# Performance work log

Measured on AMD Instinct MI355X. Metric: run time of the kernel, lower is better.

The kernel has to match this reference:

```python
import jax, jax.numpy as jnp
import numpy as np
from jax import lax

N_NODES = 50000
N_EDGES = 200000
N_FEAT = 512
HIDDEN = 256
N_FILT = 4
FIND_STEPS = 18  # > log2(N_NODES); valid because union-by-size bounds tree height


def _find(parent, x):
    # pointer-jump to root; fixed trip count, root is a fixed point (parent[r]==r)
    return lax.fori_loop(0, FIND_STEPS, lambda i, y: parent[y], x)


def persistence_dim0(v, src, dst):
    """Dim-0 persistence diagram for one filtration.
    v: (N,) node filtration values. src/dst: (E,) int32 edge endpoints.
    Returns (N, 2) array of (birth, death) pairs, one per node.
    Union-find over edges sorted by filtration value max(v[u], v[w]);
    when two components merge, the younger one's minimum node dies at the edge value.
    Essential components die at max(v). The scan is purely integer-typed so the
    only differentiable path to deaths is the final gather from edge weights w.
    """
    N = v.shape[0]
    w = jnp.maximum(v[src], v[dst])  # (E,) edge filtration values
    edge_order = lax.stop_gradient(jnp.argsort(w)).astype(jnp.int32)
    vertex_order = jnp.argsort(lax.stop_gradient(v))
    rank = jnp.zeros((N,), jnp.int32).at[vertex_order].set(jnp.arange(N, dtype=jnp.int32))

    init = (
        jnp.arange(N, dtype=jnp.int32),      # parent
        jnp.ones((N,), jnp.int32),           # component size (union by size)
        rank,                                 # min birth-rank of component, stored at root
        jnp.arange(N, dtype=jnp.int32),      # node achieving min rank, stored at root
        jnp.full((N,), -1, jnp.int32),       # killing edge index per node (-1 = essential)
    )

    def step(carry, e):
        parent, size, mrank, mnode, kill = carry
        u = src[e]
        t = dst[e]
        ru = _find(parent, u)
        rt = _find(parent, t)
        merge = ru != rt
        # younger component = larger min birth-rank; its representative node dies here
        ru_young = mrank[ru] > mrank[rt]
        young = jnp.where(ru_young, ru, rt)
        kn = mnode[young]
        kill = kill.at[kn].set(jnp.where(merge, e, kill[kn]))
        # union by size: attach smaller tree under larger
        big = jnp.where(size[ru] >= size[rt], ru, rt)
        small = jnp.where(size[ru] >= size[rt], rt, ru)
        parent = parent.at[small].set(jnp.where(merge, big, parent[small]))
        size = size.at[big].set(jnp.where(merge, size[ru] + size[rt], size[big]))
        nm_rank = jnp.minimum(mrank[ru], mrank[rt])
        nm_node = jnp.where(mrank[ru] <= mrank[rt], mnode[ru], mnode[rt])
        mrank = mrank.at[big].set(jnp.where(merge, nm_rank, mrank[big]))
        mnode = mnode.at[big].set(jnp.where(merge, nm_node, mnode[big]))
        return (parent, size, mrank, mnode, kill), None

    (_, _, _, _, kill), _ = lax.scan(step, init, edge_order)
    death = jnp.where(kill >= 0, w[jnp.maximum(kill, 0)], jnp.max(v))
    return jnp.stack([v, death], axis=-1)  # (N, 2)


def setup_inputs() -> dict:
    key = jax.random.key(0)
    k1, k2, k3, k4 = jax.random.split(key, 4)
    X = jax.random.normal(k1, (N_NODES, N_FEAT), dtype=jnp.float32)
    edge_index = jax.random.randint(k2, (2, N_EDGES), 0, N_NODES, dtype=jnp.int64)
    s1 = 1.0 / np.sqrt(N_FEAT)
    s2 = 1.0 / np.sqrt(HIDDEN)
    W1 = jax.random.uniform(k3, (N_FEAT, HIDDEN), jnp.float32, -s1, s1)
    b1 = jnp.zeros((HIDDEN,), jnp.float32)
    W2 = jax.random.uniform(k4, (HIDDEN, N_FILT), jnp.float32, -s2, s2)
    b2 = jnp.zeros((N_FILT,), jnp.float32)
    return {"X": X, "W1": W1, "b1": b1, "W2": W2, "b2": b2, "edge_index": edge_index}


def reference(X, W1, b1, W2, b2, edge_index):
    # filtration MLP: Linear -> ReLU -> Linear, (n_nodes, n_filtrations)
    filt = jax.nn.relu(X @ W1 + b1) @ W2 + b2
    src = edge_index[0].astype(jnp.int32)
    dst = edge_index[1].astype(jnp.int32)
    # (n_filtrations, n_nodes, 2) dim-0 persistence diagrams
    diagrams = jax.vmap(lambda v: persistence_dim0(v, src, dst))(filt.T)
    return diagrams
```

## Files before the change

### kernel.cpp

```cpp
#include <hip/hip_runtime.h>
#include <stdint.h>

#define NN 50000
#define NE 200000
#define NFEAT 512
#define NHID 256
#define NPART 32
#define NCB 7
#define CSTEP 25000
#define NGUF 56
#define NBLKE 196
#define NBLKN 49

typedef unsigned long long u64;
typedef unsigned int u32;
typedef unsigned short u16;

__device__ const int PB[NPART + 1] = {
    0, 6272, 12544, 18816, 25088, 31360, 37632, 43904, 50176,
    56448, 62720, 68992, 75264, 81536, 87808, 94080, 100352,
    106624, 112896, 119168, 125440, 131712, 137984, 144256, 150528,
    156800, 163072, 169344, 175616, 181888, 188160, 194432, 200000};

__device__ const int GOFF[NCB + 1] = {0, 2, 6, 12, 20, 30, 42, 56};

__device__ __forceinline__ u32 encf(float x) {
  u32 u = __float_as_uint(x);
  return (u & 0x80000000u) ? ~u : (u | 0x80000000u);
}
__device__ __forceinline__ float decf(u32 y) {
  u32 u = (y & 0x80000000u) ? (y ^ 0x80000000u) : ~y;
  return __uint_as_float(u);
}

#define SWZ(c) ((c) ^ ((((c) >> 5) & 7) << 2))

__global__ __launch_bounds__(256) void mlp_kernel(
    const float* __restrict__ X, const float* __restrict__ W1,
    const float* __restrict__ b1, const float* __restrict__ W2,
    const float* __restrict__ b2, float* __restrict__ filt)
{
  __shared__ float As[64][33];
  __shared__ float Ws[32][256];
  __shared__ float W2s[256][4];

  const int tid = threadIdx.x;
  const int row0 = blockIdx.x * 64;
  const int tr = tid >> 4, tc = tid & 15;

  for (int i = tid; i < NHID * 4; i += 256) W2s[i >> 2][i & 3] = W2[i];

  float4 acc[4][4];
  #pragma unroll
  for (int i = 0; i < 4; i++)
    #pragma unroll
    for (int q = 0; q < 4; q++) acc[i][q] = make_float4(0.f, 0.f, 0.f, 0.f);

  for (int k0 = 0; k0 < NFEAT; k0 += 32) {
    __syncthreads();
    {
      const int r = tid >> 3, c4 = (tid & 7) << 2;
      #pragma unroll
      for (int rr = 0; rr < 2; rr++) {
        const int row = r + rr * 32;
        const int grow = row0 + row;
        float4 v = make_float4(0.f, 0.f, 0.f, 0.f);
        if (grow < NN) v = *(const float4*)&X[(size_t)grow * NFEAT + k0 + c4];
        As[row][c4 + 0] = v.x; As[row][c4 + 1] = v.y;
        As[row][c4 + 2] = v.z; As[row][c4 + 3] = v.w;
      }
      const int wr = tid >> 6, wc4 = (tid & 63) << 2;
      const int pc = SWZ(wc4);
      #pragma unroll
      for (int rr = 0; rr < 8; rr++) {
        const int rowk = wr + rr * 4;
        float4 v = *(const float4*)&W1[(size_t)(k0 + rowk) * NHID + wc4];
        *(float4*)&Ws[rowk][pc] = v;
      }
    }
    __syncthreads();
    #pragma unroll 8
    for (int kk = 0; kk < 32; kk++) {
      const float a0 = As[tr * 4 + 0][kk], a1 = As[tr * 4 + 1][kk],
                  a2 = As[tr * 4 + 2][kk], a3 = As[tr * 4 + 3][kk];
      #pragma unroll
      for (int q = 0; q < 4; q++) {
        const int col = tc * 16 + q * 4;
        const float4 wv = *(const float4*)&Ws[kk][SWZ(col)];
        acc[0][q].x += a0 * wv.x; acc[0][q].y += a0 * wv.y;
        acc[0][q].z += a0 * wv.z; acc[0][q].w += a0 * wv.w;
        acc[1][q].x += a1 * wv.x; acc[1][q].y += a1 * wv.y;
        acc[1][q].z += a1 * wv.z; acc[1][q].w += a1 * wv.w;
        acc[2][q].x += a2 * wv.x; acc[2][q].y += a2 * wv.y;
        acc[2][q].z += a2 * wv.z; acc[2][q].w += a2 * wv.w;
        acc[3][q].x += a3 * wv.x; acc[3][q].y += a3 * wv.y;
        acc[3][q].w += a3 * wv.w; acc[3][q].z += a3 * wv.z;
      }
    }
  }

  float p[4][4];
  #pragma unroll
  for (int i = 0; i < 4; i++)
    #pragma unroll
    for (int f = 0; f < 4; f++) p[i][f] = 0.f;

  #pragma unroll
  for (int q = 0; q < 4; q++) {
    const int colb = tc * 16 + q * 4;
    float bb[4];
    #pragma unroll
    for (int j = 0; j < 4; j++) bb[j] = b1[colb + j];
    #pragma unroll
    for (int i = 0; i < 4; i++) {
      float h[4] = {acc[i][q].x + bb[0], acc[i][q].y + bb[1],
                    acc[i][q].z + bb[2], acc[i][q].w + bb[3]};
      #pragma unroll
      for (int j = 0; j < 4; j++) {
        const float hh = fmaxf(h[j], 0.f);
        #pragma unroll
        for (int f = 0; f < 4; f++) p[i][f] += hh * W2s[colb + j][f];
      }
    }
  }

  #pragma unroll
  for (int m = 1; m < 16; m <<= 1)
    #pragma unroll
    for (int i = 0; i < 4; i++)
      #pragma unroll
      for (int f = 0; f < 4; f++)
        p[i][f] += __shfl_xor(p[i][f], m, 64);

  if (tc == 0) {
    const float c0 = b2[0], c1 = b2[1], c2 = b2[2], c3 = b2[3];
    #pragma unroll
    for (int i = 0; i < 4; i++) {
      const int row = row0 + tr * 4 + i;
      if (row < NN) {
        float4 o = make_float4(p[i][0] + c0, p[i][1] + c1, p[i][2] + c2, p[i][3] + c3);
        *(float4*)&filt[(size_t)row * 4] = o;
      }
    }
  }
}

__global__ void zero4_kernel(u32* __restrict__ maxv) {
  if (threadIdx.x < 4) maxv[threadIdx.x] = 0u;
}

__global__ __launch_bounds__(256) void maxv_kernel(const float* __restrict__ filt,
                                                   u32* __restrict__ maxv)
{
  __shared__ u32 lm[4];
  if (threadIdx.x < 4) lm[threadIdx.x] = 0u;
  __syncthreads();
  const int n = blockIdx.x * 256 + threadIdx.x;
  if (n < NN) {
    const float4 v = *(const float4*)&filt[(size_t)n * 4];
    atomicMax(&lm[0], encf(v.x));
    atomicMax(&lm[1], encf(v.y));
    atomicMax(&lm[2], encf(v.z));
    atomicMax(&lm[3], encf(v.w));
  }
  __syncthreads();
  if (threadIdx.x < 4) atomicMax(&maxv[threadIdx.x], lm[threadIdx.x]);
}

__global__ __launch_bounds__(256) void nodeprep_kernel(const float* __restrict__ filt,
                                                       u64* __restrict__ nodekeys)
{
  const int n = blockIdx.x * 256 + threadIdx.x;
  const int f = blockIdx.y;
  if (n < NN) {
    const float v = filt[(size_t)n * 4 + f];
    nodekeys[(size_t)f * NN + n] = ((u64)encf(v) << 32) | (u32)n;
  }
}

__global__ __launch_bounds__(256) void radix_hist(
    const u64* __restrict__ src, u32* __restrict__ hist, int n, int nblk, int shift)
{
  __shared__ u32 cnt[256];
  const int tid = threadIdx.x;
  const int blk = blockIdx.x;
  const int f = blockIdx.y;
  src += (size_t)f * n;
  hist += (size_t)f * 256 * nblk;
  cnt[tid] = 0;
  __syncthreads();
  #pragma unroll
  for (int k = 0; k < 4; k++) {
    const int i = blk * 1024 + k * 256 + tid;
    if (i < n) atomicAdd(&cnt[(u32)(src[i] >> shift) & 255u], 1u);
  }
  __syncthreads();
  hist[(size_t)tid * nblk + blk] = cnt[tid];
}

__global__ __launch_bounds__(256) void radix_scan_rows(
    u32* __restrict__ hist, u32* __restrict__ rowtot, int nblk)
{
  __shared__ u32 buf[256];
  const int d = blockIdx.x, f = blockIdx.y;
  const int tid = threadIdx.x;
  u32* row = hist + ((size_t)f * 256 + d) * nblk;
  u32 v = (tid < nblk) ? row[tid] : 0u;
  buf[tid] = v;
  __syncthreads();
  for (int off = 1; off < 256; off <<= 1) {
    const u32 t = (tid >= off) ? buf[tid - off] : 0u;
    __syncthreads();
    buf[tid] += t;
    __syncthreads();
  }
  if (tid < nblk) row[tid] = buf[tid] - v;
  if (tid == 255) rowtot[f * 256 + d] = buf[255];
}

__global__ __launch_bounds__(256) void radix_scan_digits(u32* __restrict__ rowtot)
{
  __shared__ u32 buf[256];
  const int f = blockIdx.x, tid = threadIdx.x;
  const u32 v = rowtot[f * 256 + tid];
  buf[tid] = v;
  __syncthreads();
  for (int off = 1; off < 256; off <<= 1) {
    const u32 t = (tid >= off) ? buf[tid - off] : 0u;
    __syncthreads();
    buf[tid] += t;
    __syncthreads();
  }
  rowtot[f * 256 + tid] = buf[tid] - v;
}

__global__ __launch_bounds__(256) void radix_scatter(
    const u64* __restrict__ src, u64* __restrict__ dst,
    const u32* __restrict__ hist, const u32* __restrict__ rowtot,
    int n, int nblk, int shift)
{
  __shared__ u32 baseD[256];
  __shared__ u32 accum[256];
  __shared__ u32 roundCnt[4 * 256];
  const int tid = threadIdx.x;
  const int blk = blockIdx.x;
  const int f = blockIdx.y;
  const int lane = tid & 63, wid = tid >> 6;
  src += (size_t)f * n;
  dst += (size_t)f * n;
  baseD[tid] = hist[(size_t)f * 256 * nblk + (size_t)tid * nblk + blk] +
               rowtot[f * 256 + tid];
  accum[tid] = 0;
  for (int k = 0; k < 4; k++) {
    roundCnt[tid] = 0; roundCnt[tid + 256] = 0;
    roundCnt[tid + 512] = 0; roundCnt[tid + 768] = 0;
    __syncthreads();
    const int i = blk * 1024 + k * 256 + tid;
    const bool valid = (i < n);
    const u64 key = valid ? src[i] : 0ull;
    const u32 d = (u32)(key >> shift) & 255u;
    u64 peers = __ballot(valid);
    #pragma unroll
    for (int b = 0; b < 8; b++) {
      const u64 bal = __ballot((d >> b) & 1u);
      peers &= ((d >> b) & 1u) ? bal : ~bal;
    }
    const u32 rank = (u32)__popcll(peers & ((1ull << lane) - 1ull));
    if (valid && (__ffsll((long long)peers) - 1 == lane))
      roundCnt[wid * 256 + d] = (u32)__popcll(peers);
    __syncthreads();
    if (valid) {
      u32 off = baseD[d] + accum[d] + rank;
      for (int w2 = 0; w2 < wid; w2++) off += roundCnt[w2 * 256 + d];
      dst[off] = key;
    }
    __syncthreads();
    accum[tid] += roundCnt[tid] + roundCnt[256 + tid] +
                  roundCnt[512 + tid] + roundCnt[768 + tid];
    __syncthreads();
  }
}

__global__ __launch_bounds__(256) void rank_kernel(const u64* __restrict__ nodekeys,
                                                   u32* __restrict__ rankOf,
                                                   u32* __restrict__ nodeOf)
{
  const int j = blockIdx.x * 256 + threadIdx.x;
  const int f = blockIdx.y;
  if (j < NN) {
    const u64 kk = nodekeys[(size_t)f * NN + j];
    const u32 node = (u32)(kk & 0xffffffffu);
    rankOf[(size_t)f * NN + node] = (u32)j;
    nodeOf[(size_t)f * NN + j] = node;
  }
}

__global__ __launch_bounds__(256) void init_kernel(
    const float* __restrict__ filt, const u32* __restrict__ maxv,
    float* __restrict__ out)
{
  const int n = blockIdx.x * 256 + threadIdx.x;
  const int f = blockIdx.y;
  if (n < NN) {
    const size_t idx = (size_t)f * NN + n;
    out[idx * 2 + 0] = filt[(size_t)n * 4 + f];
    out[idx * 2 + 1] = decf(maxv[f]);
  }
}

__global__ __launch_bounds__(256) void prep_kernel(
    const int* __restrict__ ei, const float* __restrict__ filt,
    const u32* __restrict__ rankOf, u64* __restrict__ pairs)
{
  const int e = blockIdx.x * 256 + threadIdx.x;
  if (e >= NE) return;
  const int s = ei[e];
  const int d = ei[NE + e];
  const float4 vs = *(const float4*)&filt[(size_t)s * 4];
  const float4 vd = *(const float4*)&filt[(size_t)d * 4];
  float wf[4] = {fmaxf(vs.x, vd.x), fmaxf(vs.y, vd.y),
                 fmaxf(vs.z, vd.z), fmaxf(vs.w, vd.w)};
  #pragma unroll
  for (int f = 0; f < 4; f++) {
    const u32 ru = rankOf[(size_t)f * NN + s];
    const u32 rt = rankOf[(size_t)f * NN + d];
    pairs[(size_t)f * NE + e] = ((u64)encf(wf[f]) << 32) | ((ru << 16) | rt);
  }
}

__global__ __launch_bounds__(256) void gparinit_kernel(u32* __restrict__ gpar)
{
  const int n = blockIdx.x * 256 + threadIdx.x;
  const int jf = blockIdx.y;
  if (n < NN) gpar[(size_t)jf * NN + n] = (u32)n;
}

__global__ __launch_bounds__(1024) void guf_kernel(
    const u64* __restrict__ pairs, u32* __restrict__ gpar)
{
  const int bx = blockIdx.x;
  const int f = blockIdx.y;
  int j = 0;
  while (j < NCB - 1 && bx >= GOFF[j + 1]) j++;
  const int b = bx - GOFF[j];
  const int nb = 2 * (j + 1);
  const int cb = CSTEP * (j + 1);
  const int s0 = (int)(((long long)cb * b) / nb);
  const int s1 = (int)(((long long)cb * (b + 1)) / nb);
  u32* gp = gpar + (size_t)(j * 4 + f) * NN;
  const u64* ps = pairs + (size_t)f * NE;

  for (int e = s0 + (int)threadIdx.x; e < s1; e += 1024) {
    const u32 pr = (u32)(ps[e] & 0xffffffffu);
    u32 x = pr >> 16, y = pr & 0xffffu;
    while (true) {
      u32 px = gp[x];
      while (px != x) { const u32 g = gp[px]; gp[x] = g; x = g; px = gp[x]; }
      u32 py = gp[y];
      while (py != y) { const u32 g = gp[py]; gp[y] = g; y = g; py = gp[y]; }
      if (x == y) break;
      const u32 h = (x > y) ? x : y;
      const u32 l = x ^ y ^ h;
      const u32 old = atomicCAS(&gp[h], h, l);
      if (old == h) break;
      x = old; y = l;
    }
  }
}

__global__ __launch_bounds__(1024) void uf_kernel(
    const u64* __restrict__ pairs, const u32* __restrict__ gpar,
    u64* __restrict__ qbuf, u32* __restrict__ qcnt)
{
  __shared__ __align__(16) u16 par[NN];
  __shared__ __align__(16) u32 scratch[1024];
  const int q = blockIdx.x, f = blockIdx.y;
  const int tid = threadIdx.x;
  const u64* ps = pairs + (size_t)f * NE;
  const int lo = PB[q], hi = PB[q + 1];
  int jb = lo / CSTEP; if (jb > NCB) jb = NCB;
  const int base = jb * CSTEP;

  u32* par32 = (u32*)par;
  if (jb == 0) {
    for (int j = tid; j < NN / 2; j += 1024)
      par32[j] = ((u32)(2 * j + 1) << 16) | (u32)(2 * j);
  } else {
    const u32* gp = gpar + (size_t)((jb - 1) * 4 + f) * NN;
    for (int n = tid; n < NN; n += 1024) par[n] = (u16)gp[n];
  }
  __syncthreads();

  {
    volatile u16* vpar = par;
    for (int e = base + tid; e < lo; e += 1024) {
      const u32 pr = (u32)(ps[e] & 0xffffffffu);
      u32 x = pr >> 16, y = pr & 0xffffu;
      while (true) {
        u32 px = vpar[x];
        while (px != x) { const u32 g = vpar[px]; vpar[x] = (u16)g; x = g; px = vpar[x]; }
        u32 py = vpar[y];
        while (py != y) { const u32 g = vpar[py]; vpar[y] = (u16)g; y = g; py = vpar[y]; }
        if (x == y) break;
        const u32 h = (x > y) ? x : y;
        const u32 l = x ^ y ^ h;
        volatile u32* w32 = (volatile u32*)par32 + (h >> 1);
        const bool hiH = (h & 1u) != 0u;
        bool hooked = false, lost = false;
        while (!hooked && !lost) {
          const u32 cur = *w32;
          const u32 half = hiH ? (cur >> 16) : (cur & 0xffffu);
          if (half != h) { lost = true; break; }
          const u32 nw = hiH ? ((cur & 0x0000ffffu) | (l << 16))
                             : ((cur & 0xffff0000u) | l);
          if (atomicCAS((u32*)w32, cur, nw) == cur) hooked = true;
        }
        if (hooked) break;
        x = h; y = l;
      }
    }
  }
  __syncthreads();

  if (tid >= 64) return;
  const int lane = tid;
  u64* qb = qbuf + (size_t)f * NE + lo;
  u32 qcount = 0;
  uint4* h4 = (uint4*)scratch;
  const uint4 zz = make_uint4(0u, 0u, 0u, 0u);

  u64 pair0 = ps[lo + lane];
  u64 pair1 = (lo + 64 < hi) ? ps[lo + 64 + lane] : 0ull;

  for (int base2 = lo; base2 < hi; base2 += 64) {
    u64 pair2 = 0ull;
    if (base2 + 128 < hi) pair2 = ps[base2 + 128 + lane];

    const u32 pr = (u32)(pair0 & 0xffffffffu);
    const u32 deathw = (u32)(pair0 >> 32);
    const int u = (int)(pr >> 16), t = (int)(pr & 0xffffu);

    int ru = u, rt = t;
    u32 pu = par[ru], pt = par[rt];
    while (pu != (u32)ru || pt != (u32)rt) {
      const u32 gu = par[pu];
      const u32 gt = par[pt];
      if (pu != (u32)ru) { par[ru] = (u16)gu; ru = (int)gu; }
      if (pt != (u32)rt) { par[rt] = (u16)gt; rt = (int)gt; }
      pu = par[ru]; pt = par[rt];
    }

    const bool mg = (ru != rt);
    const u32 winv = (ru < rt) ? (u32)ru : (u32)rt;
    const u32 losev = (u32)(ru ^ rt) ^ winv;
    const u64 mball = __ballot(mg);
    const int nm = (int)__popcll(mball);

    bool flag = false;
    if (nm > 1) {
      #pragma unroll
      for (int k = 0; k < 4; k++) h4[lane + 64 * k] = zz;
      const u32 hu = ((u32)ru * 2654435761u) >> 22;
      const u32 ht = ((u32)rt * 2654435761u) >> 22;
      if (mg) { atomicAdd(&scratch[hu], 1u); atomicAdd(&scratch[ht], 1u); }
      asm volatile("s_waitcnt lgkmcnt(0)" ::: "memory");
      u32 cl = 0u;
      if (mg) cl = scratch[(losev == (u32)ru) ? hu : ht];
      flag = mg && (cl >= 2u);
    }

    u32 myLose = 0xffffffffu, myWin = 0u;
    if (mg && !flag) { myLose = losev; myWin = winv; }

    u64 chain = __ballot(flag);
    u32 mp = ((u32)ru << 16) | (u32)rt;
    while (chain) {
      const int l = __ffsll((long long)chain) - 1;
      chain &= (chain - 1);
      const u32 ab = (u32)__builtin_amdgcn_readlane((int)mp, l);
      const u32 a = ab >> 16, b = ab & 0xffffu;
      if (a != b) {
        const u32 win = a < b ? a : b;
        const u32 lose = a ^ b ^ win;
        const bool isme = (lane == l);
        myLose = isme ? lose : myLose;
        myWin = isme ? win : myWin;
        const u32 h2 = mp >> 16, l2m = mp & 0xffffu;
        mp = ((h2 == lose ? win : h2) << 16) | (l2m == lose ? win : l2m);
      }
    }

    const u64 mmask = __ballot(myLose != 0xffffffffu);
    if (myLose != 0xffffffffu) {
      par[myLose] = (u16)myWin;
      const u32 idx = (u32)__popcll(mmask & ((1ull << lane) - 1ull));
      qb[qcount + idx] = ((u64)deathw << 32) | myLose;
    }
    qcount += (u32)__popcll(mmask);

    asm volatile("s_waitcnt lgkmcnt(0)" ::: "memory");
    __builtin_amdgcn_sched_barrier(0);
    pair0 = pair1; pair1 = pair2;
  }
  if (lane == 0) qcnt[f * NPART + q] = qcount;
}

__global__ __launch_bounds__(256) void finalize_kernel(
    const u64* __restrict__ qbuf, const u32* __restrict__ qcnt,
    const u32* __restrict__ nodeOf, float* __restrict__ out)
{
  const int e = blockIdx.x * 256 + threadIdx.x;
  const int f = blockIdx.y;
  if (e >= NE) return;
  int q = 0;
  while (q < NPART - 1 && e >= PB[q + 1]) q++;
  if ((u32)(e - PB[q]) < qcnt[f * NPART + q]) {
    const u64 v = qbuf[(size_t)f * NE + e];
    const u32 lose = (u32)(v & 0xffffffffu);
    const u32 node = nodeOf[(size_t)f * NN + lose];
    out[((size_t)f * NN + node) * 2 + 1] = decf((u32)(v >> 32));
  }
}

extern "C" void kernel_launch(void* const* d_in, const int* in_sizes, int n_in,
                              void* d_out, int out_size, void* d_ws, size_t ws_size,
                              hipStream_t stream)
{
  const float* X  = (const float*)d_in[0];
  const float* W1 = (const float*)d_in[1];
  const float* b1 = (const float*)d_in[2];
  const float* W2 = (const float*)d_in[3];
  const float* b2 = (const float*)d_in[4];
  const int*   EI = (const int*)d_in[5];
  float* out = (float*)d_out;

  char* w = (char*)d_ws;
  u64*  A      = (u64*)w;   w += (size_t)4 * NE * sizeof(u64);
  char* Bb     = w;         w += (size_t)4 * NE * sizeof(u64);
  u64*  qbuf   = (u64*)w;   w += (size_t)4 * NE * sizeof(u64);
  float* filt  = (float*)w; w += (size_t)NN * 4 * sizeof(float);
  u32*  rankOf = (u32*)w;   w += (size_t)4 * NN * sizeof(u32);
  u32*  nodeOf = (u32*)w;   w += (size_t)4 * NN * sizeof(u32);
  u32*  qcnt   = (u32*)w;   w += 128 * sizeof(u32);
  u32*  rowtot = (u32*)w;   w += 4 * 256 * sizeof(u32);
  u32*  maxv   = (u32*)w;   w += 4 * sizeof(u32);

  u64* NA   = (u64*)Bb;
  u64* NB   = (u64*)(Bb + 1600000);
  u64* EB   = (u64*)Bb;
  u32* gpar = (u32*)Bb;
  u32* nhist = rankOf;
  u32* ehist = (u32*)filt;

  const size_t need = (size_t)(w - (char*)d_ws);
  if (ws_size < need) return;

  const int nodeBlocks = (NN + 255) / 256;
  const int edgeBlocks = (NE + 255) / 256;

  zero4_kernel<<<dim3(1), dim3(64), 0, stream>>>(maxv);
  mlp_kernel<<<dim3((NN + 63) / 64), dim3(256), 0, stream>>>(X, W1, b1, W2, b2, filt);
  maxv_kernel<<<dim3(nodeBlocks, 1), dim3(256), 0, stream>>>(filt, maxv);
  nodeprep_kernel<<<dim3(nodeBlocks, 4), dim3(256), 0, stream>>>(filt, NA);

  {
    u64 *s = NA, *d = NB;
    for (int p = 0; p < 4; p++) {
      const int sh = 32 + 8 * p;
      radix_hist<<<dim3(NBLKN, 4), dim3(256), 0, stream>>>(s, nhist, NN, NBLKN, sh);
      radix_scan_rows<<<dim3(256, 4), dim3(256), 0, stream>>>(nhist, rowtot, NBLKN);
      radix_scan_digits<<<dim3(4), dim3(256), 0, stream>>>(rowtot);
      radix_scatter<<<dim3(NBLKN, 4), dim3(256), 0, stream>>>(s, d, nhist, rowtot,
                                                              NN, NBLKN, sh);
      u64* t = s; s = d; d = t;
    }
  }

  rank_kernel<<<dim3(nodeBlocks, 4), dim3(256), 0, stream>>>(NA, rankOf, nodeOf);
  init_kernel<<<dim3(nodeBlocks, 4), dim3(256), 0, stream>>>(filt, maxv, out);
  prep_kernel<<<dim3(edgeBlocks, 1), dim3(256), 0, stream>>>(EI, filt, rankOf, A);

  {
    u64 *s = A, *d = EB;
    for (int p = 0; p < 4; p++) {
      const int sh = 32 + 8 * p;
      radix_hist<<<dim3(NBLKE, 4), dim3(256), 0, stream>>>(s, ehist, NE, NBLKE, sh);
      radix_scan_rows<<<dim3(256, 4), dim3(256), 0, stream>>>(ehist, rowtot, NBLKE);
      radix_scan_digits<<<dim3(4), dim3(256), 0, stream>>>(rowtot);
      radix_scatter<<<dim3(NBLKE, 4), dim3(256), 0, stream>>>(s, d, ehist, rowtot,
                                                              NE, NBLKE, sh);
      u64* t = s; s = d; d = t;
    }
  }

  gparinit_kernel<<<dim3(nodeBlocks, NCB * 4), dim3(256), 0, stream>>>(gpar);
  guf_kernel<<<dim3(NGUF, 4), dim3(1024), 0, stream>>>(A, gpar);

  uf_kernel<<<dim3(NPART, 4), dim3(1024), 0, stream>>>(A, gpar, qbuf, qcnt);

  finalize_kernel<<<dim3(edgeBlocks, 4), dim3(256), 0, stream>>>(qbuf, qcnt, nodeOf, out);
}
```

Before: 1.259 ms.

## Build checkpoint union-find forests incrementally instead of from scratch

Each of the NCB checkpoint parent arrays used to be built independently by one kernel that replayed every edge from zero up to its checkpoint. Now checkpoint j starts as a copy of checkpoint j-1 and only unions the edges in its own CSTEP chunk. This cuts total union work from quadratic to linear in the number of checkpoints. The cost is 14 serialized launches instead of 2 and less parallelism per launch (8x4 blocks).

```diff
diff --git a/kernel.cpp b/kernel.cpp
--- a/kernel.cpp
+++ b/kernel.cpp
@@ -8,7 +8,6 @@
 #define NPART 32
 #define NCB 7
 #define CSTEP 25000
-#define NGUF 56
 #define NBLKE 196
 #define NBLKN 49
 
@@ -21,8 +20,6 @@
     56448, 62720, 68992, 75264, 81536, 87808, 94080, 100352,
     106624, 112896, 119168, 125440, 131712, 137984, 144256, 150528,
     156800, 163072, 169344, 175616, 181888, 188160, 194432, 200000};
-
-__device__ const int GOFF[NCB + 1] = {0, 2, 6, 12, 20, 30, 42, 56};
 
 __device__ __forceinline__ u32 encf(float x) {
   u32 u = __float_as_uint(x);
@@ -328,29 +325,25 @@
   }
 }
 
-__global__ __launch_bounds__(256) void gparinit_kernel(u32* __restrict__ gpar)
+__global__ __launch_bounds__(256) void gcopy_kernel(u32* __restrict__ gpar, int j)
 {
   const int n = blockIdx.x * 256 + threadIdx.x;
-  const int jf = blockIdx.y;
-  if (n < NN) gpar[(size_t)jf * NN + n] = (u32)n;
-}
-
-__global__ __launch_bounds__(1024) void guf_kernel(
-    const u64* __restrict__ pairs, u32* __restrict__ gpar)
-{
-  const int bx = blockIdx.x;
-  const int f = blockIdx.y;
-  int j = 0;
-  while (j < NCB - 1 && bx >= GOFF[j + 1]) j++;
-  const int b = bx - GOFF[j];
-  const int nb = 2 * (j + 1);
-  const int cb = CSTEP * (j + 1);
-  const int s0 = (int)(((long long)cb * b) / nb);
-  const int s1 = (int)(((long long)cb * (b + 1)) / nb);
+  const int f = blockIdx.y;
+  if (n < NN) {
+    u32* dst = gpar + (size_t)(j * 4 + f) * NN;
+    dst[n] = (j == 0) ? (u32)n : gpar[(size_t)((j - 1) * 4 + f) * NN + n];
+  }
+}
+
+__global__ __launch_bounds__(1024) void gufc_kernel(
+    const u64* __restrict__ pairs, u32* __restrict__ gpar, int j)
+{
+  const int f = blockIdx.y;
   u32* gp = gpar + (size_t)(j * 4 + f) * NN;
   const u64* ps = pairs + (size_t)f * NE;
-
-  for (int e = s0 + (int)threadIdx.x; e < s1; e += 1024) {
+  const int lo = CSTEP * j, hi = CSTEP * (j + 1);
+
+  for (int e = lo + blockIdx.x * 1024 + threadIdx.x; e < hi; e += gridDim.x * 1024) {
     const u32 pr = (u32)(ps[e] & 0xffffffffu);
     u32 x = pr >> 16, y = pr & 0xffffu;
     while (true) {
@@ -593,8 +586,10 @@
     }
   }
 
-  gparinit_kernel<<<dim3(nodeBlocks, NCB * 4), dim3(256), 0, stream>>>(gpar);
-  guf_kernel<<<dim3(NGUF, 4), dim3(1024), 0, stream>>>(A, gpar);
+  for (int j = 0; j < NCB; j++) {
+    gcopy_kernel<<<dim3(nodeBlocks, 4), dim3(256), 0, stream>>>(gpar, j);
+    gufc_kernel<<<dim3(8, 4), dim3(1024), 0, stream>>>(A, gpar, j);
+  }
 
   uf_kernel<<<dim3(NPART, 4), dim3(1024), 0, stream>>>(A, gpar, qbuf, qcnt);
 
```

Result: no change. 1.270 ms (+0.9%).
